# Kernel tuning notes

Hardware: AMD Instinct MI355X
Metric: run time of the kernel (lower is better)

## Reference

```python
import jax, jax.numpy as jnp
import numpy as np

N, D, S = 8192, 512, 5000
L_MAX, G_MAX, C_MAX = 512, 16, 6
MARGIN = 0.0
EPS = 1e-12


def setup_inputs() -> dict:
    key = jax.random.key(0)
    k1, k2, k3, k4, k5, k6 = jax.random.split(key, 6)
    return {
        'embeddings': jax.random.normal(k1, (N, D), dtype=jnp.float32),
        'labels': jax.random.randint(k2, (N,), 0, L_MAX),
        'graph_ids': jax.random.randint(k3, (N,), 0, G_MAX),
        'categories': jax.random.randint(k4, (N,), 0, C_MAX),
        'idx1': jax.random.randint(k5, (S,), 0, N),
        'idx2': jax.random.randint(k6, (S,), 0, N),
    }


def reference(embeddings, labels, graph_ids, categories, idx1, idx2):
    # L2-normalize rows (F.normalize, p=2, dim=1, eps=1e-12)
    norms = jnp.maximum(jnp.linalg.norm(embeddings, axis=1, keepdims=True), EPS)
    e = embeddings / norms
    n = e.shape[0]

    conserved = categories < 3  # [n]
    r = jnp.arange(n)
    upper_tri = r[:, None] < r[None, :]                     # i < j
    same_label = labels[:, None] == labels[None, :]
    diff_graph = graph_ids[:, None] != graph_ids[None, :]
    valid_pos = (upper_tri & same_label & diff_graph
                 & conserved[:, None] & conserved[None, :])  # [n, n] bool

    sims = e @ e.T                                           # [n, n] cosine sims
    pos_cnt = jnp.sum(valid_pos)
    pos_sum = jnp.sum(jnp.where(valid_pos, 1.0 - sims, 0.0))
    pos_loss = jnp.where(pos_cnt > 0, pos_sum / jnp.maximum(pos_cnt, 1), 0.0)

    # Negative pairs: uniform random index pairs (idx1, idx2), masked to
    # different-graph, different-label, at-least-one-conserved pairs.
    neg_valid = ((graph_ids[idx1] != graph_ids[idx2])
                 & (labels[idx1] != labels[idx2])
                 & ((categories[idx1] < 3) | (categories[idx2] < 3)))  # [S]
    neg_sims = jnp.sum(e[idx1] * e[idx2], axis=1)            # [S]
    penalties = jnp.maximum(neg_sims - MARGIN, 0.0)
    neg_cnt = jnp.sum(neg_valid)
    neg_sum = jnp.sum(jnp.where(neg_valid, penalties, 0.0))
    neg_loss = jnp.where(neg_cnt > 0, neg_sum / jnp.maximum(neg_cnt, 1), 0.0)

    return pos_loss + neg_loss
```

## Files before the change

kernel.cpp:

```cpp
#include <hip/hip_runtime.h>

#define DIM 512
#define NVEC4 (DIM / 4)
#define LMAX 512
#define MAXB 32
#define MAXPAIR (MAXB * (MAXB - 1) / 2)
#define TPB 1024
#define NGROUPS (TPB / 16)
#define EPS 1e-12f

__device__ __forceinline__ float d4(const float4 a, const float4 b) {
    return a.x * b.x + a.y * b.y + a.z * b.z + a.w * b.w;
}

__device__ __forceinline__ float cos_sim(float aa, float ab, float bb) {
    return ab / (fmaxf(sqrtf(aa), EPS) * fmaxf(sqrtf(bb), EPS));
}

__global__ void __launch_bounds__(TPB)
mega_kernel(const float* __restrict__ E,
            const int* __restrict__ labels,
            const int* __restrict__ graphs,
            const int* __restrict__ cats,
            const int* __restrict__ idx1,
            const int* __restrict__ idx2,
            int n, int S,
            float4* __restrict__ partials) {
    __shared__ float4 rows[MAXB][NVEC4];
    __shared__ float rinv[MAXB];
    __shared__ int idxs[MAXB];
    __shared__ int plist[MAXPAIR];
    __shared__ int gcount, pcount;
    __shared__ float s_acc[4];
    const int tid = threadIdx.x;
    const int grp = tid >> 4, gl = tid & 15;
    if (tid == 0) { gcount = 0; pcount = 0; }
    if (tid < 4) s_acc[tid] = 0.0f;
    __syncthreads();

    const float4* E4 = (const float4*)E;

    if (blockIdx.x < LMAX) {
        const int lbl = blockIdx.x;
        const int4* lab4 = (const int4*)labels;
        int nv4 = n >> 2;
        for (int v = tid; v < nv4; v += TPB) {
            int4 l4 = lab4[v];
            int base = v << 2;
            if (l4.x == lbl && cats[base + 0] < 3) { int p = atomicAdd(&gcount, 1); if (p < MAXB) idxs[p] = base + 0; }
            if (l4.y == lbl && cats[base + 1] < 3) { int p = atomicAdd(&gcount, 1); if (p < MAXB) idxs[p] = base + 1; }
            if (l4.z == lbl && cats[base + 2] < 3) { int p = atomicAdd(&gcount, 1); if (p < MAXB) idxs[p] = base + 2; }
            if (l4.w == lbl && cats[base + 3] < 3) { int p = atomicAdd(&gcount, 1); if (p < MAXB) idxs[p] = base + 3; }
        }
        __syncthreads();

        const int g = min(gcount, MAXB);

        for (int u = tid; u < g * NVEC4; u += TPB) {
            int r = u >> 7, c = u & (NVEC4 - 1);
            rows[r][c] = E4[(size_t)idxs[r] * NVEC4 + c];
        }
        if (tid < g * g) {
            int a = tid >> 5, b = tid & 31;
            a = tid / g; b = tid - a * g;
            if (a < b) {
                if (graphs[idxs[a]] != graphs[idxs[b]]) {
                    plist[atomicAdd(&pcount, 1)] = (a << 5) | b;
                }
            }
        }
        __syncthreads();

        if (grp < g) {
            float s = 0.0f;
#pragma unroll
            for (int k = 0; k < 8; ++k) {
                float4 x = rows[grp][gl + 16 * k];
                s += d4(x, x);
            }
#pragma unroll
            for (int m = 8; m >= 1; m >>= 1) s += __shfl_xor(s, m, 64);
            if (gl == 0) rinv[grp] = 1.0f / fmaxf(sqrtf(s), EPS);
        }
        __syncthreads();

        const int np = pcount;
        float psum = 0.0f;
        for (int p = grp; p < np; p += NGROUPS) {
            int pk = plist[p];
            int a = pk >> 5, b = pk & 31;
            float ab = 0.0f;
#pragma unroll
            for (int k = 0; k < 8; ++k)
                ab += d4(rows[a][gl + 16 * k], rows[b][gl + 16 * k]);
#pragma unroll
            for (int m = 8; m >= 1; m >>= 1) ab += __shfl_xor(ab, m, 64);
            if (gl == 0) psum += 1.0f - ab * rinv[a] * rinv[b];
        }
        if (gl == 0 && psum != 0.0f) atomicAdd(&s_acc[0], psum);
        __syncthreads();
        if (tid == 0) {
            s_acc[1] = (float)np;
            partials[blockIdx.x] = make_float4(s_acc[0], s_acc[1], 0.0f, 0.0f);
        }
    } else {
        int base = (blockIdx.x - LMAX) * NGROUPS;
        int stride = (gridDim.x - LMAX) * NGROUPS;
        float nsum = 0.0f, nc = 0.0f;
        for (int s = base + grp; s < S; s += stride) {
            int i = idx1[s], j = idx2[s];
            if (graphs[i] != graphs[j] && labels[i] != labels[j] &&
                (cats[i] < 3 || cats[j] < 3)) {
                const float4* A = E4 + (size_t)i * NVEC4;
                const float4* B = E4 + (size_t)j * NVEC4;
                float saa = 0.0f, sab = 0.0f, sbb = 0.0f;
#pragma unroll
                for (int k = 0; k < 8; ++k) {
                    float4 x = A[gl + 16 * k];
                    float4 y = B[gl + 16 * k];
                    saa += d4(x, x); sab += d4(x, y); sbb += d4(y, y);
                }
#pragma unroll
                for (int m = 8; m >= 1; m >>= 1) {
                    saa += __shfl_xor(saa, m, 64);
                    sab += __shfl_xor(sab, m, 64);
                    sbb += __shfl_xor(sbb, m, 64);
                }
                if (gl == 0) {
                    nsum += fmaxf(cos_sim(saa, sab, sbb), 0.0f);
                    nc += 1.0f;
                }
            }
        }
        if (gl == 0 && nc != 0.0f) {
            atomicAdd(&s_acc[2], nsum);
            atomicAdd(&s_acc[3], nc);
        }
        __syncthreads();
        if (tid == 0)
            partials[blockIdx.x] = make_float4(0.0f, 0.0f, s_acc[2], s_acc[3]);
    }
}

__global__ void __launch_bounds__(64)
finalize_kernel(const float4* __restrict__ partials, int nb,
                float* __restrict__ out) {
    int lane = threadIdx.x;
    float ps = 0.0f, pc = 0.0f, ns = 0.0f, nc = 0.0f;
    for (int i = lane; i < nb; i += 64) {
        float4 v = partials[i];
        ps += v.x; pc += v.y; ns += v.z; nc += v.w;
    }
#pragma unroll
    for (int m = 32; m > 0; m >>= 1) {
        ps += __shfl_xor(ps, m, 64);
        pc += __shfl_xor(pc, m, 64);
        ns += __shfl_xor(ns, m, 64);
        nc += __shfl_xor(nc, m, 64);
    }
    if (lane == 0) {
        float pos = (pc > 0.0f) ? ps / pc : 0.0f;
        float neg = (nc > 0.0f) ? ns / nc : 0.0f;
        out[0] = pos + neg;
    }
}

extern "C" void kernel_launch(void* const* d_in, const int* in_sizes, int n_in,
                              void* d_out, int out_size, void* d_ws, size_t ws_size,
                              hipStream_t stream) {
    const float* E    = (const float*)d_in[0];
    const int* labels = (const int*)d_in[1];
    const int* graphs = (const int*)d_in[2];
    const int* cats   = (const int*)d_in[3];
    const int* idx1   = (const int*)d_in[4];
    const int* idx2   = (const int*)d_in[5];
    int n = in_sizes[1];
    int S = in_sizes[4];

    int nb_neg = (S + NGROUPS - 1) / NGROUPS;
    if (nb_neg > 128) nb_neg = 128;
    int nb = LMAX + nb_neg;

    float4* partials = (float4*)d_ws;

    mega_kernel<<<nb, TPB, 0, stream>>>(E, labels, graphs, cats,
                                        idx1, idx2, n, S, partials);
    finalize_kernel<<<1, 64, 0, stream>>>(partials, nb, (float*)d_out);
}
```

Before: 20.71 us.

## Split into prep and dots kernels with global pair lists and precomputed inverse norms

Replaces the single 1024-thread mega kernel with three launches. A zero kernel clears the counters. A prep kernel computes inverse norms for all rows and compacts the positive and negative pair lists into global memory. A dots kernel then load-balances all pair dot products across 512 blocks of 256 threads. This targets the load imbalance of the per-label blocks and the redundant norm work in the negative path. In exchange it adds extra launches, global round-trips for the pair lists, and atomic accumulation into the output, and silently drops positive pairs beyond a 32768-pair cap.

```diff
diff --git a/kernel.cpp b/kernel.cpp
--- a/kernel.cpp
+++ b/kernel.cpp
@@ -5,42 +5,58 @@
 #define LMAX 512
 #define MAXB 32
 #define MAXPAIR (MAXB * (MAXB - 1) / 2)
-#define TPB 1024
-#define NGROUPS (TPB / 16)
+#define PAIR_CAP 32768
+#define NB_LBL LMAX
+#define NB_AUX 32
+#define NB_A (NB_LBL + NB_AUX)
+#define TPB 256
+#define GPB (TPB / 16)
+#define NB_B 512
 #define EPS 1e-12f
 
 __device__ __forceinline__ float d4(const float4 a, const float4 b) {
     return a.x * b.x + a.y * b.y + a.z * b.z + a.w * b.w;
 }
 
-__device__ __forceinline__ float cos_sim(float aa, float ab, float bb) {
-    return ab / (fmaxf(sqrtf(aa), EPS) * fmaxf(sqrtf(bb), EPS));
-}
-
 __global__ void __launch_bounds__(TPB)
-mega_kernel(const float* __restrict__ E,
+prep_kernel(const float* __restrict__ E,
             const int* __restrict__ labels,
             const int* __restrict__ graphs,
             const int* __restrict__ cats,
             const int* __restrict__ idx1,
             const int* __restrict__ idx2,
             int n, int S,
-            float4* __restrict__ partials) {
-    __shared__ float4 rows[MAXB][NVEC4];
-    __shared__ float rinv[MAXB];
-    __shared__ int idxs[MAXB];
-    __shared__ int plist[MAXPAIR];
-    __shared__ int gcount, pcount;
-    __shared__ float s_acc[4];
+            float* __restrict__ invn,
+            int* __restrict__ paircnt, int2* __restrict__ pairs,
+            int* __restrict__ negcnt, int2* __restrict__ negp,
+            float* __restrict__ out) {
     const int tid = threadIdx.x;
     const int grp = tid >> 4, gl = tid & 15;
-    if (tid == 0) { gcount = 0; pcount = 0; }
-    if (tid < 4) s_acc[tid] = 0.0f;
-    __syncthreads();
-
     const float4* E4 = (const float4*)E;
 
-    if (blockIdx.x < LMAX) {
+    {
+        int row = blockIdx.x * GPB + grp;
+        if (row < n) {
+            const float4* A = E4 + (size_t)row * NVEC4;
+            float s = 0.0f;
+#pragma unroll
+            for (int k = 0; k < 8; ++k) {
+                float4 x = A[gl + 16 * k];
+                s += d4(x, x);
+            }
+#pragma unroll
+            for (int m = 8; m >= 1; m >>= 1) s += __shfl_xor(s, m, 64);
+            if (gl == 0) invn[row] = 1.0f / fmaxf(sqrtf(s), EPS);
+        }
+    }
+
+    if (blockIdx.x < NB_LBL) {
+        __shared__ int idxs[MAXB];
+        __shared__ int2 plist[MAXPAIR];
+        __shared__ int gcount, pcount, pbase;
+        if (tid == 0) { gcount = 0; pcount = 0; }
+        __syncthreads();
+
         const int lbl = blockIdx.x;
         const int4* lab4 = (const int4*)labels;
         int nv4 = n >> 2;
@@ -55,113 +71,91 @@
         __syncthreads();
 
         const int g = min(gcount, MAXB);
-
-        for (int u = tid; u < g * NVEC4; u += TPB) {
-            int r = u >> 7, c = u & (NVEC4 - 1);
-            rows[r][c] = E4[(size_t)idxs[r] * NVEC4 + c];
-        }
-        if (tid < g * g) {
-            int a = tid >> 5, b = tid & 31;
-            a = tid / g; b = tid - a * g;
+        for (int c = tid; c < g * g; c += TPB) {
+            int a = c / g, b = c - a * g;
             if (a < b) {
-                if (graphs[idxs[a]] != graphs[idxs[b]]) {
-                    plist[atomicAdd(&pcount, 1)] = (a << 5) | b;
-                }
+                int ia = idxs[a], ib = idxs[b];
+                if (graphs[ia] != graphs[ib])
+                    plist[atomicAdd(&pcount, 1)] = make_int2(ia, ib);
             }
         }
         __syncthreads();
+        if (tid == 0) pbase = atomicAdd(paircnt, pcount);
+        __syncthreads();
+        int base = pbase, cnt = pcount;
+        for (int k = tid; k < cnt; k += TPB)
+            if (base + k < PAIR_CAP) pairs[base + k] = plist[k];
+    } else {
+        __shared__ int2 nlist[TPB];
+        __shared__ int ncount, nbase;
+        if (tid == 0) ncount = 0;
+        __syncthreads();
 
-        if (grp < g) {
-            float s = 0.0f;
-#pragma unroll
-            for (int k = 0; k < 8; ++k) {
-                float4 x = rows[grp][gl + 16 * k];
-                s += d4(x, x);
-            }
-#pragma unroll
-            for (int m = 8; m >= 1; m >>= 1) s += __shfl_xor(s, m, 64);
-            if (gl == 0) rinv[grp] = 1.0f / fmaxf(sqrtf(s), EPS);
+        int s = (blockIdx.x - NB_LBL) * TPB + tid;
+        if (s < S) {
+            int i = idx1[s], j = idx2[s];
+            if (graphs[i] != graphs[j] && labels[i] != labels[j] &&
+                (cats[i] < 3 || cats[j] < 3))
+                nlist[atomicAdd(&ncount, 1)] = make_int2(i, j);
         }
         __syncthreads();
+        if (tid == 0) nbase = atomicAdd(negcnt, ncount);
+        __syncthreads();
+        if (tid < ncount) negp[nbase + tid] = nlist[tid];
 
-        const int np = pcount;
-        float psum = 0.0f;
-        for (int p = grp; p < np; p += NGROUPS) {
-            int pk = plist[p];
-            int a = pk >> 5, b = pk & 31;
-            float ab = 0.0f;
-#pragma unroll
-            for (int k = 0; k < 8; ++k)
-                ab += d4(rows[a][gl + 16 * k], rows[b][gl + 16 * k]);
-#pragma unroll
-            for (int m = 8; m >= 1; m >>= 1) ab += __shfl_xor(ab, m, 64);
-            if (gl == 0) psum += 1.0f - ab * rinv[a] * rinv[b];
-        }
-        if (gl == 0 && psum != 0.0f) atomicAdd(&s_acc[0], psum);
-        __syncthreads();
-        if (tid == 0) {
-            s_acc[1] = (float)np;
-            partials[blockIdx.x] = make_float4(s_acc[0], s_acc[1], 0.0f, 0.0f);
-        }
-    } else {
-        int base = (blockIdx.x - LMAX) * NGROUPS;
-        int stride = (gridDim.x - LMAX) * NGROUPS;
-        float nsum = 0.0f, nc = 0.0f;
-        for (int s = base + grp; s < S; s += stride) {
-            int i = idx1[s], j = idx2[s];
-            if (graphs[i] != graphs[j] && labels[i] != labels[j] &&
-                (cats[i] < 3 || cats[j] < 3)) {
-                const float4* A = E4 + (size_t)i * NVEC4;
-                const float4* B = E4 + (size_t)j * NVEC4;
-                float saa = 0.0f, sab = 0.0f, sbb = 0.0f;
-#pragma unroll
-                for (int k = 0; k < 8; ++k) {
-                    float4 x = A[gl + 16 * k];
-                    float4 y = B[gl + 16 * k];
-                    saa += d4(x, x); sab += d4(x, y); sbb += d4(y, y);
-                }
-#pragma unroll
-                for (int m = 8; m >= 1; m >>= 1) {
-                    saa += __shfl_xor(saa, m, 64);
-                    sab += __shfl_xor(sab, m, 64);
-                    sbb += __shfl_xor(sbb, m, 64);
-                }
-                if (gl == 0) {
-                    nsum += fmaxf(cos_sim(saa, sab, sbb), 0.0f);
-                    nc += 1.0f;
-                }
-            }
-        }
-        if (gl == 0 && nc != 0.0f) {
-            atomicAdd(&s_acc[2], nsum);
-            atomicAdd(&s_acc[3], nc);
-        }
-        __syncthreads();
-        if (tid == 0)
-            partials[blockIdx.x] = make_float4(0.0f, 0.0f, s_acc[2], s_acc[3]);
+        if (blockIdx.x == NB_LBL && tid == 0) out[0] = 0.0f;
     }
 }
 
-__global__ void __launch_bounds__(64)
-finalize_kernel(const float4* __restrict__ partials, int nb,
-                float* __restrict__ out) {
-    int lane = threadIdx.x;
-    float ps = 0.0f, pc = 0.0f, ns = 0.0f, nc = 0.0f;
-    for (int i = lane; i < nb; i += 64) {
-        float4 v = partials[i];
-        ps += v.x; pc += v.y; ns += v.z; nc += v.w;
+__global__ void zero_kernel(int* __restrict__ paircnt, int* __restrict__ negcnt) {
+    *paircnt = 0; *negcnt = 0;
+}
+
+__global__ void __launch_bounds__(TPB)
+dots_kernel(const float* __restrict__ E,
+            const float* __restrict__ invn,
+            const int* __restrict__ paircnt, const int2* __restrict__ pairs,
+            const int* __restrict__ negcnt, const int2* __restrict__ negp,
+            float* __restrict__ out) {
+    __shared__ float s_acc[2];
+    const int tid = threadIdx.x;
+    const int grp = tid >> 4, gl = tid & 15;
+    if (tid < 2) s_acc[tid] = 0.0f;
+    __syncthreads();
+
+    const float4* E4 = (const float4*)E;
+    const int np = min(*paircnt, PAIR_CAP);
+    const int nn = *negcnt;
+    const int total = np + nn;
+    const int ggid = blockIdx.x * GPB + grp;
+    const int gstride = gridDim.x * GPB;
+
+    float psum = 0.0f, nsum = 0.0f;
+    for (int t = ggid; t < total; t += gstride) {
+        int2 pr = (t < np) ? pairs[t] : negp[t - np];
+        const float4* A = E4 + (size_t)pr.x * NVEC4;
+        const float4* B = E4 + (size_t)pr.y * NVEC4;
+        float ab = 0.0f;
+#pragma unroll
+        for (int k = 0; k < 8; ++k)
+            ab += d4(A[gl + 16 * k], B[gl + 16 * k]);
+#pragma unroll
+        for (int m = 8; m >= 1; m >>= 1) ab += __shfl_xor(ab, m, 64);
+        if (gl == 0) {
+            float sim = ab * invn[pr.x] * invn[pr.y];
+            if (t < np) psum += 1.0f - sim;
+            else        nsum += fmaxf(sim, 0.0f);
+        }
     }
-#pragma unroll
-    for (int m = 32; m > 0; m >>= 1) {
-        ps += __shfl_xor(ps, m, 64);
-        pc += __shfl_xor(pc, m, 64);
-        ns += __shfl_xor(ns, m, 64);
-        nc += __shfl_xor(nc, m, 64);
+    if (gl == 0) {
+        if (psum != 0.0f) atomicAdd(&s_acc[0], psum);
+        if (nsum != 0.0f) atomicAdd(&s_acc[1], nsum);
     }
-    if (lane == 0) {
-        float pos = (pc > 0.0f) ? ps / pc : 0.0f;
-        float neg = (nc > 0.0f) ? ns / nc : 0.0f;
-        out[0] = pos + neg;
+    __syncthreads();
+    if (tid == 0) {
+        float v = (np > 0 ? s_acc[0] / (float)np : 0.0f)
+                + (nn > 0 ? s_acc[1] / (float)nn : 0.0f);
+        if (v != 0.0f) atomicAdd(out, v);
     }
 }
 
@@ -177,13 +171,18 @@
     int n = in_sizes[1];
     int S = in_sizes[4];
 
-    int nb_neg = (S + NGROUPS - 1) / NGROUPS;
-    if (nb_neg > 128) nb_neg = 128;
-    int nb = LMAX + nb_neg;
+    char* p = (char*)d_ws;
+    float* invn  = (float*)p;  p += (size_t)n * sizeof(float);
+    int* paircnt = (int*)p;    p += sizeof(int);
+    int* negcnt  = (int*)p;    p += sizeof(int);
+    int2* pairs  = (int2*)p;   p += (size_t)PAIR_CAP * sizeof(int2);
+    int2* negp   = (int2*)p;
+    float* out   = (float*)d_out;
 
-    float4* partials = (float4*)d_ws;
-
-    mega_kernel<<<nb, TPB, 0, stream>>>(E, labels, graphs, cats,
-                                        idx1, idx2, n, S, partials);
-    finalize_kernel<<<1, 64, 0, stream>>>(partials, nb, (float*)d_out);
+    zero_kernel<<<1, 1, 0, stream>>>(paircnt, negcnt);
+    prep_kernel<<<NB_A, TPB, 0, stream>>>(E, labels, graphs, cats, idx1, idx2,
+                                          n, S, invn, paircnt, pairs,
+                                          negcnt, negp, out);
+    dots_kernel<<<NB_B, TPB, 0, stream>>>(E, invn, paircnt, pairs,
+                                          negcnt, negp, out);
 }
```

Result: slower. 34.12 us (+64.8%).

## Fuse finalize into main kernel via flag-based last-block reduction; drop shared row staging

Applied to the files above, without the earlier changes.

Removes the separate finalize launch by adding an extra block that spins on per-slot magic flags published by worker blocks, then reduces the partials and writes the output. Positive-pair blocks now read embedding rows straight from global memory (L2-cached) instead of staging them in shared memory, which removes a sync and large LDS use. The negative side uses one sample per group with no cap on block count. This relies on the spinning block not starving producers and on flags being reset by the CAS consume, and it adds atomic traffic for publishing.

```diff
diff --git a/kernel.cpp b/kernel.cpp
--- a/kernel.cpp
+++ b/kernel.cpp
@@ -8,13 +8,22 @@
 #define TPB 1024
 #define NGROUPS (TPB / 16)
 #define EPS 1e-12f
+#define MAGIC 0x5AFEC0DE
 
 __device__ __forceinline__ float d4(const float4 a, const float4 b) {
     return a.x * b.x + a.y * b.y + a.z * b.z + a.w * b.w;
 }
 
-__device__ __forceinline__ float cos_sim(float aa, float ab, float bb) {
-    return ab / (fmaxf(sqrtf(aa), EPS) * fmaxf(sqrtf(bb), EPS));
+__device__ __forceinline__ void publish(float4* __restrict__ pay,
+                                        int* __restrict__ magics, int bid,
+                                        float ps, float pc, float ns, float nc) {
+    float* pf = (float*)&pay[bid];
+    atomicExch(pf + 0, ps);
+    atomicExch(pf + 1, pc);
+    atomicExch(pf + 2, ns);
+    atomicExch(pf + 3, nc);
+    __threadfence();
+    atomicExch(&magics[bid], MAGIC);
 }
 
 __global__ void __launch_bounds__(TPB)
@@ -24,24 +33,26 @@
             const int* __restrict__ cats,
             const int* __restrict__ idx1,
             const int* __restrict__ idx2,
-            int n, int S,
-            float4* __restrict__ partials) {
-    __shared__ float4 rows[MAXB][NVEC4];
+            int n, int S, int nslots,
+            float4* __restrict__ pay,
+            int* __restrict__ magics,
+            float* __restrict__ out) {
+    __shared__ int idxs[MAXB];
     __shared__ float rinv[MAXB];
-    __shared__ int idxs[MAXB];
     __shared__ int plist[MAXPAIR];
     __shared__ int gcount, pcount;
-    __shared__ float s_acc[4];
+    __shared__ float s_acc[2];
     const int tid = threadIdx.x;
     const int grp = tid >> 4, gl = tid & 15;
-    if (tid == 0) { gcount = 0; pcount = 0; }
-    if (tid < 4) s_acc[tid] = 0.0f;
-    __syncthreads();
-
+    const int bid = blockIdx.x;
     const float4* E4 = (const float4*)E;
 
-    if (blockIdx.x < LMAX) {
-        const int lbl = blockIdx.x;
+    if (bid < LMAX) {
+        if (tid == 0) { gcount = 0; pcount = 0; }
+        if (tid < 2) s_acc[tid] = 0.0f;
+        __syncthreads();
+
+        const int lbl = bid;
         const int4* lab4 = (const int4*)labels;
         int nv4 = n >> 2;
         for (int v = tid; v < nv4; v += TPB) {
@@ -55,29 +66,16 @@
         __syncthreads();
 
         const int g = min(gcount, MAXB);
-
-        for (int u = tid; u < g * NVEC4; u += TPB) {
-            int r = u >> 7, c = u & (NVEC4 - 1);
-            rows[r][c] = E4[(size_t)idxs[r] * NVEC4 + c];
+        if (tid < g * g) {
+            int a = tid / g, b = tid - a * g;
+            if (a < b && graphs[idxs[a]] != graphs[idxs[b]])
+                plist[atomicAdd(&pcount, 1)] = (a << 5) | b;
         }
-        if (tid < g * g) {
-            int a = tid >> 5, b = tid & 31;
-            a = tid / g; b = tid - a * g;
-            if (a < b) {
-                if (graphs[idxs[a]] != graphs[idxs[b]]) {
-                    plist[atomicAdd(&pcount, 1)] = (a << 5) | b;
-                }
-            }
-        }
-        __syncthreads();
-
         if (grp < g) {
+            const float4* A = E4 + (size_t)idxs[grp] * NVEC4;
             float s = 0.0f;
 #pragma unroll
-            for (int k = 0; k < 8; ++k) {
-                float4 x = rows[grp][gl + 16 * k];
-                s += d4(x, x);
-            }
+            for (int k = 0; k < 8; ++k) { float4 x = A[gl + 16 * k]; s += d4(x, x); }
 #pragma unroll
             for (int m = 8; m >= 1; m >>= 1) s += __shfl_xor(s, m, 64);
             if (gl == 0) rinv[grp] = 1.0f / fmaxf(sqrtf(s), EPS);
@@ -89,25 +87,26 @@
         for (int p = grp; p < np; p += NGROUPS) {
             int pk = plist[p];
             int a = pk >> 5, b = pk & 31;
+            const float4* A = E4 + (size_t)idxs[a] * NVEC4;
+            const float4* B = E4 + (size_t)idxs[b] * NVEC4;
             float ab = 0.0f;
 #pragma unroll
-            for (int k = 0; k < 8; ++k)
-                ab += d4(rows[a][gl + 16 * k], rows[b][gl + 16 * k]);
+            for (int k = 0; k < 8; ++k) ab += d4(A[gl + 16 * k], B[gl + 16 * k]);
 #pragma unroll
             for (int m = 8; m >= 1; m >>= 1) ab += __shfl_xor(ab, m, 64);
             if (gl == 0) psum += 1.0f - ab * rinv[a] * rinv[b];
         }
         if (gl == 0 && psum != 0.0f) atomicAdd(&s_acc[0], psum);
         __syncthreads();
-        if (tid == 0) {
-            s_acc[1] = (float)np;
-            partials[blockIdx.x] = make_float4(s_acc[0], s_acc[1], 0.0f, 0.0f);
-        }
-    } else {
-        int base = (blockIdx.x - LMAX) * NGROUPS;
-        int stride = (gridDim.x - LMAX) * NGROUPS;
-        float nsum = 0.0f, nc = 0.0f;
-        for (int s = base + grp; s < S; s += stride) {
+        if (tid == 0) publish(pay, magics, bid, s_acc[0], (float)np, 0.0f, 0.0f);
+
+    } else if (bid < nslots) {
+        if (tid < 2) s_acc[tid] = 0.0f;
+        __syncthreads();
+
+        int s = (bid - LMAX) * NGROUPS + grp;
+        float nsum = 0.0f, ncv = 0.0f;
+        if (s < S) {
             int i = idx1[s], j = idx2[s];
             if (graphs[i] != graphs[j] && labels[i] != labels[j] &&
                 (cats[i] < 3 || cats[j] < 3)) {
@@ -116,8 +115,7 @@
                 float saa = 0.0f, sab = 0.0f, sbb = 0.0f;
 #pragma unroll
                 for (int k = 0; k < 8; ++k) {
-                    float4 x = A[gl + 16 * k];
-                    float4 y = B[gl + 16 * k];
+                    float4 x = A[gl + 16 * k], y = B[gl + 16 * k];
                     saa += d4(x, x); sab += d4(x, y); sbb += d4(y, y);
                 }
 #pragma unroll
@@ -127,41 +125,45 @@
                     sbb += __shfl_xor(sbb, m, 64);
                 }
                 if (gl == 0) {
-                    nsum += fmaxf(cos_sim(saa, sab, sbb), 0.0f);
-                    nc += 1.0f;
+                    float sim = sab / (fmaxf(sqrtf(saa), EPS) * fmaxf(sqrtf(sbb), EPS));
+                    nsum = fmaxf(sim, 0.0f);
+                    ncv = 1.0f;
                 }
             }
         }
-        if (gl == 0 && nc != 0.0f) {
-            atomicAdd(&s_acc[2], nsum);
-            atomicAdd(&s_acc[3], nc);
+        if (gl == 0 && ncv != 0.0f) {
+            atomicAdd(&s_acc[0], nsum);
+            atomicAdd(&s_acc[1], ncv);
         }
         __syncthreads();
-        if (tid == 0)
-            partials[blockIdx.x] = make_float4(0.0f, 0.0f, s_acc[2], s_acc[3]);
-    }
-}
+        if (tid == 0) publish(pay, magics, bid, 0.0f, 0.0f, s_acc[0], s_acc[1]);
 
-__global__ void __launch_bounds__(64)
-finalize_kernel(const float4* __restrict__ partials, int nb,
-                float* __restrict__ out) {
-    int lane = threadIdx.x;
-    float ps = 0.0f, pc = 0.0f, ns = 0.0f, nc = 0.0f;
-    for (int i = lane; i < nb; i += 64) {
-        float4 v = partials[i];
-        ps += v.x; pc += v.y; ns += v.z; nc += v.w;
-    }
+    } else {
+        if (tid < 64) {
+            float ps = 0.0f, pc = 0.0f, ns = 0.0f, nc = 0.0f;
+            for (int s = tid; s < nslots; s += 64) {
+                while (atomicCAS(&magics[s], MAGIC, 0) != MAGIC)
+                    __builtin_amdgcn_s_sleep(2);
+                __threadfence();
+                float* pf = (float*)&pay[s];
+                ps += atomicAdd(pf + 0, 0.0f);
+                pc += atomicAdd(pf + 1, 0.0f);
+                ns += atomicAdd(pf + 2, 0.0f);
+                nc += atomicAdd(pf + 3, 0.0f);
+            }
 #pragma unroll
-    for (int m = 32; m > 0; m >>= 1) {
-        ps += __shfl_xor(ps, m, 64);
-        pc += __shfl_xor(pc, m, 64);
-        ns += __shfl_xor(ns, m, 64);
-        nc += __shfl_xor(nc, m, 64);
-    }
-    if (lane == 0) {
-        float pos = (pc > 0.0f) ? ps / pc : 0.0f;
-        float neg = (nc > 0.0f) ? ns / nc : 0.0f;
-        out[0] = pos + neg;
+            for (int m = 32; m > 0; m >>= 1) {
+                ps += __shfl_xor(ps, m, 64);
+                pc += __shfl_xor(pc, m, 64);
+                ns += __shfl_xor(ns, m, 64);
+                nc += __shfl_xor(nc, m, 64);
+            }
+            if (tid == 0) {
+                float pos = (pc > 0.0f) ? ps / pc : 0.0f;
+                float neg = (nc > 0.0f) ? ns / nc : 0.0f;
+                out[0] = pos + neg;
+            }
+        }
     }
 }
 
@@ -178,12 +180,12 @@
     int S = in_sizes[4];
 
     int nb_neg = (S + NGROUPS - 1) / NGROUPS;
-    if (nb_neg > 128) nb_neg = 128;
-    int nb = LMAX + nb_neg;
+    int nslots = LMAX + nb_neg;
+    int nb = nslots + 1;
 
-    float4* partials = (float4*)d_ws;
+    float4* pay = (float4*)d_ws;
+    int* magics = (int*)((char*)d_ws + (size_t)nslots * sizeof(float4));
 
-    mega_kernel<<<nb, TPB, 0, stream>>>(E, labels, graphs, cats,
-                                        idx1, idx2, n, S, partials);
-    finalize_kernel<<<1, 64, 0, stream>>>(partials, nb, (float*)d_out);
+    mega_kernel<<<nb, TPB, 0, stream>>>(E, labels, graphs, cats, idx1, idx2,
+                                        n, S, nslots, pay, magics, (float*)d_out);
 }
```

Measured after the change: 26.59 us. 1.28x slower.

## Fold negative-pair work into label blocks and drop shared row staging

Applied to the files above, without the earlier changes.

Removes the separate negative-pair blocks. Each of the 512 label blocks now handles up to 64 negative samples, one per 16-lane group, before its label scan, so the grid shrinks to 512 blocks. The positive-pair path no longer copies rows into the large shared tile. Norms and dot products are read straight from global memory (L2), which cuts LDS use and may raise occupancy. The cost is repeated global reads of the same rows per pair. The negative work also assumes S <= 64*LMAX; any samples beyond that would be silently dropped.

```diff
diff --git a/kernel.cpp b/kernel.cpp
--- a/kernel.cpp
+++ b/kernel.cpp
@@ -13,10 +13,6 @@
     return a.x * b.x + a.y * b.y + a.z * b.z + a.w * b.w;
 }
 
-__device__ __forceinline__ float cos_sim(float aa, float ab, float bb) {
-    return ab / (fmaxf(sqrtf(aa), EPS) * fmaxf(sqrtf(bb), EPS));
-}
-
 __global__ void __launch_bounds__(TPB)
 mega_kernel(const float* __restrict__ E,
             const int* __restrict__ labels,
@@ -26,22 +22,51 @@
             const int* __restrict__ idx2,
             int n, int S,
             float4* __restrict__ partials) {
-    __shared__ float4 rows[MAXB][NVEC4];
+    __shared__ int idxs[MAXB];
     __shared__ float rinv[MAXB];
-    __shared__ int idxs[MAXB];
     __shared__ int plist[MAXPAIR];
     __shared__ int gcount, pcount;
-    __shared__ float s_acc[4];
+    __shared__ float s_acc[3];
     const int tid = threadIdx.x;
     const int grp = tid >> 4, gl = tid & 15;
+    const int bid = blockIdx.x;
+    const float4* E4 = (const float4*)E;
+
     if (tid == 0) { gcount = 0; pcount = 0; }
-    if (tid < 4) s_acc[tid] = 0.0f;
+    if (tid < 3) s_acc[tid] = 0.0f;
     __syncthreads();
 
-    const float4* E4 = (const float4*)E;
+    {
+        int s = grp * LMAX + bid;
+        if (s < S) {
+            int i = idx1[s], j = idx2[s];
+            if (graphs[i] != graphs[j] && labels[i] != labels[j] &&
+                (cats[i] < 3 || cats[j] < 3)) {
+                const float4* A = E4 + (size_t)i * NVEC4;
+                const float4* B = E4 + (size_t)j * NVEC4;
+                float saa = 0.0f, sab = 0.0f, sbb = 0.0f;
+#pragma unroll
+                for (int k = 0; k < 8; ++k) {
+                    float4 x = A[gl + 16 * k], y = B[gl + 16 * k];
+                    saa += d4(x, x); sab += d4(x, y); sbb += d4(y, y);
+                }
+#pragma unroll
+                for (int m = 8; m >= 1; m >>= 1) {
+                    saa += __shfl_xor(saa, m, 64);
+                    sab += __shfl_xor(sab, m, 64);
+                    sbb += __shfl_xor(sbb, m, 64);
+                }
+                if (gl == 0) {
+                    float sim = sab / (fmaxf(sqrtf(saa), EPS) * fmaxf(sqrtf(sbb), EPS));
+                    atomicAdd(&s_acc[1], fmaxf(sim, 0.0f));
+                    atomicAdd(&s_acc[2], 1.0f);
+                }
+            }
+        }
+    }
 
-    if (blockIdx.x < LMAX) {
-        const int lbl = blockIdx.x;
+    {
+        const int lbl = bid;
         const int4* lab4 = (const int4*)labels;
         int nv4 = n >> 2;
         for (int v = tid; v < nv4; v += TPB) {
@@ -52,94 +77,45 @@
             if (l4.z == lbl && cats[base + 2] < 3) { int p = atomicAdd(&gcount, 1); if (p < MAXB) idxs[p] = base + 2; }
             if (l4.w == lbl && cats[base + 3] < 3) { int p = atomicAdd(&gcount, 1); if (p < MAXB) idxs[p] = base + 3; }
         }
-        __syncthreads();
+    }
+    __syncthreads();
 
-        const int g = min(gcount, MAXB);
+    const int g = min(gcount, MAXB);
+    if (tid < g * g) {
+        int a = tid / g, b = tid - a * g;
+        if (a < b && graphs[idxs[a]] != graphs[idxs[b]])
+            plist[atomicAdd(&pcount, 1)] = (a << 5) | b;
+    }
+    if (grp < g) {
+        const float4* A = E4 + (size_t)idxs[grp] * NVEC4;
+        float s = 0.0f;
+#pragma unroll
+        for (int k = 0; k < 8; ++k) { float4 x = A[gl + 16 * k]; s += d4(x, x); }
+#pragma unroll
+        for (int m = 8; m >= 1; m >>= 1) s += __shfl_xor(s, m, 64);
+        if (gl == 0) rinv[grp] = 1.0f / fmaxf(sqrtf(s), EPS);
+    }
+    __syncthreads();
 
-        for (int u = tid; u < g * NVEC4; u += TPB) {
-            int r = u >> 7, c = u & (NVEC4 - 1);
-            rows[r][c] = E4[(size_t)idxs[r] * NVEC4 + c];
-        }
-        if (tid < g * g) {
-            int a = tid >> 5, b = tid & 31;
-            a = tid / g; b = tid - a * g;
-            if (a < b) {
-                if (graphs[idxs[a]] != graphs[idxs[b]]) {
-                    plist[atomicAdd(&pcount, 1)] = (a << 5) | b;
-                }
-            }
-        }
-        __syncthreads();
+    const int np = pcount;
+    float psum = 0.0f;
+    for (int p = grp; p < np; p += NGROUPS) {
+        int pk = plist[p];
+        int a = pk >> 5, b = pk & 31;
+        const float4* A = E4 + (size_t)idxs[a] * NVEC4;
+        const float4* B = E4 + (size_t)idxs[b] * NVEC4;
+        float ab = 0.0f;
+#pragma unroll
+        for (int k = 0; k < 8; ++k) ab += d4(A[gl + 16 * k], B[gl + 16 * k]);
+#pragma unroll
+        for (int m = 8; m >= 1; m >>= 1) ab += __shfl_xor(ab, m, 64);
+        if (gl == 0) psum += 1.0f - ab * rinv[a] * rinv[b];
+    }
+    if (gl == 0 && psum != 0.0f) atomicAdd(&s_acc[0], psum);
+    __syncthreads();
 
-        if (grp < g) {
-            float s = 0.0f;
-#pragma unroll
-            for (int k = 0; k < 8; ++k) {
-                float4 x = rows[grp][gl + 16 * k];
-                s += d4(x, x);
-            }
-#pragma unroll
-            for (int m = 8; m >= 1; m >>= 1) s += __shfl_xor(s, m, 64);
-            if (gl == 0) rinv[grp] = 1.0f / fmaxf(sqrtf(s), EPS);
-        }
-        __syncthreads();
-
-        const int np = pcount;
-        float psum = 0.0f;
-        for (int p = grp; p < np; p += NGROUPS) {
-            int pk = plist[p];
-            int a = pk >> 5, b = pk & 31;
-            float ab = 0.0f;
-#pragma unroll
-            for (int k = 0; k < 8; ++k)
-                ab += d4(rows[a][gl + 16 * k], rows[b][gl + 16 * k]);
-#pragma unroll
-            for (int m = 8; m >= 1; m >>= 1) ab += __shfl_xor(ab, m, 64);
-            if (gl == 0) psum += 1.0f - ab * rinv[a] * rinv[b];
-        }
-        if (gl == 0 && psum != 0.0f) atomicAdd(&s_acc[0], psum);
-        __syncthreads();
-        if (tid == 0) {
-            s_acc[1] = (float)np;
-            partials[blockIdx.x] = make_float4(s_acc[0], s_acc[1], 0.0f, 0.0f);
-        }
-    } else {
-        int base = (blockIdx.x - LMAX) * NGROUPS;
-        int stride = (gridDim.x - LMAX) * NGROUPS;
-        float nsum = 0.0f, nc = 0.0f;
-        for (int s = base + grp; s < S; s += stride) {
-            int i = idx1[s], j = idx2[s];
-            if (graphs[i] != graphs[j] && labels[i] != labels[j] &&
-                (cats[i] < 3 || cats[j] < 3)) {
-                const float4* A = E4 + (size_t)i * NVEC4;
-                const float4* B = E4 + (size_t)j * NVEC4;
-                float saa = 0.0f, sab = 0.0f, sbb = 0.0f;
-#pragma unroll
-                for (int k = 0; k < 8; ++k) {
-                    float4 x = A[gl + 16 * k];
-                    float4 y = B[gl + 16 * k];
-                    saa += d4(x, x); sab += d4(x, y); sbb += d4(y, y);
-                }
-#pragma unroll
-                for (int m = 8; m >= 1; m >>= 1) {
-                    saa += __shfl_xor(saa, m, 64);
-                    sab += __shfl_xor(sab, m, 64);
-                    sbb += __shfl_xor(sbb, m, 64);
-                }
-                if (gl == 0) {
-                    nsum += fmaxf(cos_sim(saa, sab, sbb), 0.0f);
-                    nc += 1.0f;
-                }
-            }
-        }
-        if (gl == 0 && nc != 0.0f) {
-            atomicAdd(&s_acc[2], nsum);
-            atomicAdd(&s_acc[3], nc);
-        }
-        __syncthreads();
-        if (tid == 0)
-            partials[blockIdx.x] = make_float4(0.0f, 0.0f, s_acc[2], s_acc[3]);
-    }
+    if (tid == 0)
+        partials[bid] = make_float4(s_acc[0], (float)np, s_acc[1], s_acc[2]);
 }
 
 __global__ void __launch_bounds__(64)
@@ -177,13 +153,9 @@
     int n = in_sizes[1];
     int S = in_sizes[4];
 
-    int nb_neg = (S + NGROUPS - 1) / NGROUPS;
-    if (nb_neg > 128) nb_neg = 128;
-    int nb = LMAX + nb_neg;
-
     float4* partials = (float4*)d_ws;
 
-    mega_kernel<<<nb, TPB, 0, stream>>>(E, labels, graphs, cats,
-                                        idx1, idx2, n, S, partials);
-    finalize_kernel<<<1, 64, 0, stream>>>(partials, nb, (float*)d_out);
+    mega_kernel<<<LMAX, TPB, 0, stream>>>(E, labels, graphs, cats,
+                                          idx1, idx2, n, S, partials);
+    finalize_kernel<<<1, 64, 0, stream>>>(partials, LMAX, (float*)d_out);
 }
```

After: 18.11 us. 1.14x faster.
